# Performance work log

Hardware: AMD Instinct MI355X
Metric: run time of the kernel (lower is better)

## Reference

```python
import jax, jax.numpy as jnp
import numpy as np

# Hyperparameters from __init__ defaults / chosen init kwargs
GAMMA_NEG = 4.0
GAMMA_POS = 1.0
CLIP = 0.05
EPS = 1e-8
ALPHA1 = 2.0
ALPHA_OTHER = 0.5
TOP_K = 10

B, C = 2048, 9605


def setup_inputs() -> dict:
    key = jax.random.key(0)
    k_x, k_y, k_c, k_r, k_d, k_o = jax.random.split(key, 6)
    x = jax.random.normal(k_x, (B, C), dtype=jnp.float32)
    y = (jax.random.uniform(k_y, (B, C)) < 0.01).astype(jnp.float32)
    compost_idx = jax.random.randint(k_c, (30,), 0, C, dtype=jnp.int32)
    recycle_idx = jax.random.randint(k_r, (70,), 0, C, dtype=jnp.int32)
    donate_idx = jax.random.randint(k_d, (70,), 0, C, dtype=jnp.int32)
    other_idx = jax.random.randint(k_o, (40,), 0, C, dtype=jnp.int32)
    # dense whitelist mapping: 0 = not in W_human mapping; priority compost>recycle>donate
    wl_map = jnp.zeros((C,), dtype=jnp.int32)
    wl_map = wl_map.at[other_idx].set(4)
    wl_map = wl_map.at[donate_idx].set(3)
    wl_map = wl_map.at[recycle_idx].set(2)
    wl_map = wl_map.at[compost_idx].set(1)
    return {"x": x, "y": y, "compost_idx": compost_idx,
            "recycle_idx": recycle_idx, "donate_idx": donate_idx,
            "wl_map": wl_map}


def reference(x, y, compost_idx, recycle_idx, donate_idx, wl_map):
    b, c = x.shape
    xs_pos = jax.nn.sigmoid(x)
    xs_neg = jnp.minimum(1.0 - xs_pos + CLIP, 1.0)  # clip shift, clamp max=1
    # base asymmetric BCE term: y*log(p) + (1-y)*log(1-p+clip)
    base = (y * jnp.log(jnp.maximum(xs_pos, EPS))
            + (1.0 - y) * jnp.log(jnp.maximum(xs_neg, EPS)))  # [B, C]

    # per-sample ground-truth whitelist groups (find_gt_whitelist)
    has1 = jnp.sum(y[:, compost_idx], axis=1) > 0  # [B]
    has2 = jnp.sum(y[:, recycle_idx], axis=1) > 0
    has3 = jnp.sum(y[:, donate_idx], axis=1) > 0
    gt_only4 = ~(has1 | has2 | has3)  # gt_whitelist == [4]

    # top-10 predicted classes (argsort descending, first 10)
    _, top_idx = jax.lax.top_k(xs_pos, TOP_K)  # [B, 10]
    rows = jnp.arange(b)

    def step(carry, j):
        # j: [B] class index at current rank; sequential over rank (order matters)
        mult, found = carry
        wl = wl_map[j]                      # group id of this class, 0 if unmapped
        in_map = wl > 0
        in_gt = (((wl == 1) & has1) | ((wl == 2) & has2)
                 | ((wl == 3) & has3) | ((wl == 4) & gt_only4))
        f = jnp.where(in_map & gt_only4, ALPHA_OTHER, 1.0)
        f = f * jnp.where(in_map & (~in_gt) & (~found), ALPHA1, 1.0)
        mult = mult.at[rows, j].multiply(f)
        found = found | (in_map & in_gt)
        return (mult, found), None

    init = (jnp.ones((b, c), x.dtype), jnp.zeros((b,), dtype=bool))
    (mult, found), _ = jax.lax.scan(step, init, top_idx.T)  # scan over 10 ranks

    # if no gt-whitelist match found in top-10: multiply all top-10 by alpha1 again
    extra = jnp.where(found[:, None], 1.0, ALPHA1)  # [B, 1]
    mult = mult.at[rows[:, None], top_idx].multiply(
        jnp.broadcast_to(extra, (b, TOP_K)))

    # asymmetric focal weighting (computed without grad in original)
    pt = xs_pos * y + xs_neg * (1.0 - y)
    gamma = GAMMA_POS * y + GAMMA_NEG * (1.0 - y)
    w = jax.lax.stop_gradient(jnp.power(1.0 - pt, gamma))

    return -jnp.sum(base * mult * w)
```

## Files before the change

### kernel.cpp

```cpp
#include <hip/hip_runtime.h>

#define TOPK 10
#define CLIP 0.05f
#define EPSV 1e-8f
#define ALPHA1 2.0f
#define ALPHA_OTHER 0.5f
#define TCAND 2.5f
#define MAXC 128

__device__ __forceinline__ unsigned long long pack_vc(float v, int c, int C) {
  unsigned u = __float_as_uint(v);
  unsigned key = (u & 0x80000000u) ? ~u : (u | 0x80000000u);
  return ((unsigned long long)key << 32) | (unsigned)(C - c);
}
__device__ __forceinline__ float unpack_v(unsigned long long p) {
  unsigned key = (unsigned)(p >> 32);
  unsigned u = (key & 0x80000000u) ? (key & 0x7fffffffu) : ~key;
  return __uint_as_float(u);
}
__device__ __forceinline__ int unpack_c(unsigned long long p, int C) {
  return C - (int)(unsigned)(p & 0xffffffffu);
}

__device__ __forceinline__ float base_w(float xv, bool pos) {
  float e = __expf(-xv);
  float p = __builtin_amdgcn_rcpf(1.f + e);
  float xneg = fminf(1.f - p + CLIP, 1.f);
  float q = pos ? p : xneg;
  float b = __logf(fmaxf(q, EPSV));
  float t = 1.f - q;
  float t2 = t * t;
  float w = pos ? t : t2 * t2;
  return b * w;
}

__device__ __forceinline__ void push_cand(float v, long flat, int C, double invC,
                                          int* __restrict__ cnt,
                                          unsigned long long* __restrict__ cand,
                                          int maxc) {
  int row = (int)((double)flat * invC);
  int col = (int)(flat - (long)row * (long)C);
  if (col >= C) { row++; col -= C; }
  if (col < 0)  { row--; col += C; }
  int i = atomicAdd(&cnt[row], 1);
  if (i < maxc) cand[(long)row * maxc + i] = pack_vc(v, col, C);
}

__device__ __forceinline__ void proc4(float4 X, float4 Y, float4& acc,
                                      unsigned& cmask, int slot) {
  acc.x += base_w(X.x, Y.x > 0.5f);
  acc.y += base_w(X.y, Y.y > 0.5f);
  acc.z += base_w(X.z, Y.z > 0.5f);
  acc.w += base_w(X.w, Y.w > 0.5f);
  float mx = fmaxf(fmaxf(X.x, X.y), fmaxf(X.z, X.w));
  cmask |= (mx > TCAND ? 1u : 0u) << slot;
}

__global__ __launch_bounds__(256) void stream_kernel(
    const float* __restrict__ x, const float* __restrict__ y,
    float* __restrict__ out, int* __restrict__ cnt,
    unsigned long long* __restrict__ cand, long N, int C, double invC, int maxc)
{
  const long N4 = N >> 2;
  const long S = (long)gridDim.x * 256;
  const long gtid = (long)blockIdx.x * 256 + threadIdx.x;
  const float4* __restrict__ x4 = (const float4*)x;
  const float4* __restrict__ y4 = (const float4*)y;

  float4 a0 = make_float4(0.f, 0.f, 0.f, 0.f);
  float4 a1 = make_float4(0.f, 0.f, 0.f, 0.f);
  float4 a2 = make_float4(0.f, 0.f, 0.f, 0.f);
  float4 a3 = make_float4(0.f, 0.f, 0.f, 0.f);
  unsigned cmask = 0;

  int k = 0;
  long i = gtid;
  for (; i + 3 * S < N4; i += 4 * S, k += 4) {
    float4 X0 = x4[i];         float4 Y0 = y4[i];
    float4 X1 = x4[i + S];     float4 Y1 = y4[i + S];
    float4 X2 = x4[i + 2 * S]; float4 Y2 = y4[i + 2 * S];
    float4 X3 = x4[i + 3 * S]; float4 Y3 = y4[i + 3 * S];
    proc4(X0, Y0, a0, cmask, k + 0);
    proc4(X1, Y1, a1, cmask, k + 1);
    proc4(X2, Y2, a2, cmask, k + 2);
    proc4(X3, Y3, a3, cmask, k + 3);
  }
  for (; i < N4; i += S, k++) {
    float4 X = x4[i]; float4 Y = y4[i];
    proc4(X, Y, a0, cmask, k);
  }
  float sum = (a0.x + a0.y + a0.z + a0.w) + (a1.x + a1.y + a1.z + a1.w)
            + (a2.x + a2.y + a2.z + a2.w) + (a3.x + a3.y + a3.z + a3.w);
  if (gtid == 0) {
    for (long j = N4 * 4; j < N; j++) {
      float xv = x[j];
      sum += base_w(xv, y[j] > 0.5f);
      if (xv > TCAND) push_cand(xv, j, C, invC, cnt, cand, maxc);
    }
  }

  while (cmask) {
    int b = __ffs(cmask) - 1;
    cmask &= cmask - 1;
    long ii = gtid + (long)b * S;
    float4 X = x4[ii];
    long fb = 4 * ii;
    if (X.x > TCAND) push_cand(X.x, fb + 0, C, invC, cnt, cand, maxc);
    if (X.y > TCAND) push_cand(X.y, fb + 1, C, invC, cnt, cand, maxc);
    if (X.z > TCAND) push_cand(X.z, fb + 2, C, invC, cnt, cand, maxc);
    if (X.w > TCAND) push_cand(X.w, fb + 3, C, invC, cnt, cand, maxc);
  }

#pragma unroll
  for (int off = 32; off > 0; off >>= 1) sum += __shfl_xor(sum, off, 64);
  __shared__ float s_sum[4];
  const int lane = threadIdx.x & 63, wave = threadIdx.x >> 6;
  if (lane == 0) s_sum[wave] = sum;
  __syncthreads();
  if (threadIdx.x == 0)
    atomicAdd(out, -(s_sum[0] + s_sum[1] + s_sum[2] + s_sum[3]));
}

__global__ __launch_bounds__(256) void fix_kernel(
    const float* __restrict__ x, const float* __restrict__ y,
    const int* __restrict__ compost, const int* __restrict__ recycle,
    const int* __restrict__ donate, const int* __restrict__ wl_map,
    float* __restrict__ out, const int* __restrict__ cnt,
    const unsigned long long* __restrict__ cand,
    int C, int n1, int n2, int n3, int maxc)
{
  const int row = blockIdx.x;
  const float* xr = x + (size_t)row * (size_t)C;
  const float* yr = y + (size_t)row * (size_t)C;
  const int tid = threadIdx.x;
  const int lane = tid & 63;
  const int wave = tid >> 6;

  __shared__ int s_has[3];
  __shared__ unsigned long long s_top[TOPK];

  if (tid < 3) s_has[tid] = 0;
  __syncthreads();

  const int ntot = n1 + n2 + n3;
  if (wave > 0) {
    for (int i = tid - 64; i < ntot; i += 192) {
      int which, colI;
      if (i < n1)           { which = 0; colI = compost[i]; }
      else if (i < n1 + n2) { which = 1; colI = recycle[i - n1]; }
      else                  { which = 2; colI = donate[i - n1 - n2]; }
      if (yr[colI] > 0.5f) s_has[which] = 1;
    }
  }

  if (wave == 0) {
    const int c = cnt[row];
    unsigned long long ls[TOPK];
#pragma unroll
    for (int s = 0; s < TOPK; s++) ls[s] = 0ULL;

#define INSERT(P)                                                          \
    do {                                                                   \
      unsigned long long _p = (P);                                         \
      if (_p > ls[TOPK - 1]) {                                             \
        _Pragma("unroll")                                                  \
        for (int _s = 0; _s < TOPK; _s++) {                                \
          bool _g = _p > ls[_s];                                           \
          unsigned long long _t = _g ? ls[_s] : _p;                        \
          ls[_s] = _g ? _p : ls[_s];                                       \
          _p = _t;                                                         \
        }                                                                  \
      }                                                                    \
    } while (0)

    if (c >= TOPK && c <= maxc) {
      const unsigned long long* cr = cand + (long)row * maxc;
      for (int i = lane; i < c; i += 64) INSERT(cr[i]);
    } else {
      for (int col = lane; col < C; col += 64) INSERT(pack_vc(xr[col], col, C));
    }
#undef INSERT

    for (int r = 0; r < TOPK; r++) {
      unsigned long long mine = ls[0];
      unsigned long long best = mine;
#pragma unroll
      for (int off = 32; off > 0; off >>= 1) {
        unsigned long long o = __shfl_xor(best, off, 64);
        best = (o > best) ? o : best;
      }
      if (lane == 0) s_top[r] = best;
      if (mine == best) {
#pragma unroll
        for (int s = 0; s < TOPK - 1; s++) ls[s] = ls[s + 1];
        ls[TOPK - 1] = 0ULL;
      }
    }
  }
  __syncthreads();

  if (tid == 0) {
    const bool h1 = s_has[0] != 0, h2 = s_has[1] != 0, h3 = s_has[2] != 0;
    const bool gt4 = !(h1 || h2 || h3);

    bool found = false;
    float fr[TOPK];
#pragma unroll
    for (int r = 0; r < TOPK; r++) {
      int col = unpack_c(s_top[r], C);
      int wl = wl_map[col];
      bool in_map = wl > 0;
      bool in_gt = (wl == 1 && h1) || (wl == 2 && h2) ||
                   (wl == 3 && h3) || (wl == 4 && gt4);
      float f = 1.f;
      if (in_map && gt4) f *= ALPHA_OTHER;
      if (in_map && !in_gt && !found) f *= ALPHA1;
      fr[r] = f;
      found = found || (in_map && in_gt);
    }
    const float extra = found ? 1.f : ALPHA1;
    float total = 0.f;
#pragma unroll
    for (int r = 0; r < TOPK; r++) {
      float mult = fr[r] * extra;
      if (mult != 1.f) {
        int col = unpack_c(s_top[r], C);
        float xv = unpack_v(s_top[r]);
        total += (mult - 1.f) * base_w(xv, yr[col] > 0.5f);
      }
    }
    if (total != 0.f) atomicAdd(out, -total);
  }
}

extern "C" void kernel_launch(void* const* d_in, const int* in_sizes, int n_in,
                              void* d_out, int out_size, void* d_ws, size_t ws_size,
                              hipStream_t stream) {
  const float* x       = (const float*)d_in[0];
  const float* y       = (const float*)d_in[1];
  const int*   compost = (const int*)d_in[2];
  const int*   recycle = (const int*)d_in[3];
  const int*   donate  = (const int*)d_in[4];
  const int*   wl_map  = (const int*)d_in[5];
  float* out = (float*)d_out;

  const int C  = in_sizes[5];
  const int B  = in_sizes[0] / C;
  const long N = (long)in_sizes[0];
  const int n1 = in_sizes[2], n2 = in_sizes[3], n3 = in_sizes[4];

  size_t cand_off = ((size_t)B * 4 + 7) & ~(size_t)7;
  int maxc = MAXC;
  if (ws_size < cand_off + (size_t)B * maxc * 8) {
    size_t fit = (ws_size > cand_off) ? (ws_size - cand_off) / ((size_t)B * 8) : 0;
    maxc = (int)fit;
  }
  int* cnt = (int*)d_ws;
  unsigned long long* cand = (unsigned long long*)((char*)d_ws + cand_off);
  double invC = 1.0 / (double)C;

  long N4 = N >> 2;
  long g = (N4 + 256L * 8 - 1) / (256L * 8);
  if (g < 256) g = 256;
  if (g > 16384) g = 16384;

  hipMemsetAsync(out, 0, sizeof(float), stream);
  hipMemsetAsync(cnt, 0, (size_t)B * 4, stream);
  stream_kernel<<<(int)g, 256, 0, stream>>>(x, y, out, cnt, cand, N, C, invC, maxc);
  fix_kernel<<<B, 256, 0, stream>>>(x, y, compost, recycle, donate, wl_map,
                                    out, cnt, cand, C, n1, n2, n3, maxc);
}
```

Measured before the change: 242.6 us.

## Stream inputs via direct global-to-LDS async loads with per-wave prefetch

```diff
diff --git a/kernel.cpp b/kernel.cpp
--- a/kernel.cpp
+++ b/kernel.cpp
@@ -7,6 +7,16 @@
 #define ALPHA_OTHER 0.5f
 #define TCAND 2.5f
 #define MAXC 128
+
+#define AS1 __attribute__((address_space(1)))
+#define AS3 __attribute__((address_space(3)))
+
+__device__ __forceinline__ void gl_lds16(const void* g, void* l) {
+  __builtin_amdgcn_global_load_lds((AS1 void*)(size_t)g, (AS3 void*)(size_t)l,
+                                   16, 0, 0);
+}
+#define WAIT_VM2() __builtin_amdgcn_s_waitcnt(0x0F72)
+#define WAIT_VM0() __builtin_amdgcn_s_waitcnt(0x0F70)
 
 __device__ __forceinline__ unsigned long long pack_vc(float v, int c, int C) {
   unsigned u = __float_as_uint(v);
@@ -46,76 +56,95 @@
   if (i < maxc) cand[(long)row * maxc + i] = pack_vc(v, col, C);
 }
 
-__device__ __forceinline__ void proc4(float4 X, float4 Y, float4& acc,
-                                      unsigned& cmask, int slot) {
-  acc.x += base_w(X.x, Y.x > 0.5f);
-  acc.y += base_w(X.y, Y.y > 0.5f);
-  acc.z += base_w(X.z, Y.z > 0.5f);
-  acc.w += base_w(X.w, Y.w > 0.5f);
-  float mx = fmaxf(fmaxf(X.x, X.y), fmaxf(X.z, X.w));
-  cmask |= (mx > TCAND ? 1u : 0u) << slot;
-}
-
 __global__ __launch_bounds__(256) void stream_kernel(
     const float* __restrict__ x, const float* __restrict__ y,
     float* __restrict__ out, int* __restrict__ cnt,
     unsigned long long* __restrict__ cand, long N, int C, double invC, int maxc)
 {
   const long N4 = N >> 2;
-  const long S = (long)gridDim.x * 256;
-  const long gtid = (long)blockIdx.x * 256 + threadIdx.x;
+  const long nstage = N4 >> 6;
+  const int lane = threadIdx.x & 63;
+  const int wv = threadIdx.x >> 6;
+  const long w = (long)blockIdx.x * 4 + wv;
+  const long W = (long)gridDim.x * 4;
+
   const float4* __restrict__ x4 = (const float4*)x;
   const float4* __restrict__ y4 = (const float4*)y;
 
-  float4 a0 = make_float4(0.f, 0.f, 0.f, 0.f);
-  float4 a1 = make_float4(0.f, 0.f, 0.f, 0.f);
-  float4 a2 = make_float4(0.f, 0.f, 0.f, 0.f);
-  float4 a3 = make_float4(0.f, 0.f, 0.f, 0.f);
+  __shared__ float4 sbuf[4][4][2][64];
+
+  float4 acc = make_float4(0.f, 0.f, 0.f, 0.f);
   unsigned cmask = 0;
-
-  int k = 0;
-  long i = gtid;
-  for (; i + 3 * S < N4; i += 4 * S, k += 4) {
-    float4 X0 = x4[i];         float4 Y0 = y4[i];
-    float4 X1 = x4[i + S];     float4 Y1 = y4[i + S];
-    float4 X2 = x4[i + 2 * S]; float4 Y2 = y4[i + 2 * S];
-    float4 X3 = x4[i + 3 * S]; float4 Y3 = y4[i + 3 * S];
-    proc4(X0, Y0, a0, cmask, k + 0);
-    proc4(X1, Y1, a1, cmask, k + 1);
-    proc4(X2, Y2, a2, cmask, k + 2);
-    proc4(X3, Y3, a3, cmask, k + 3);
-  }
-  for (; i < N4; i += S, k++) {
-    float4 X = x4[i]; float4 Y = y4[i];
-    proc4(X, Y, a0, cmask, k);
-  }
-  float sum = (a0.x + a0.y + a0.z + a0.w) + (a1.x + a1.y + a1.z + a1.w)
-            + (a2.x + a2.y + a2.z + a2.w) + (a3.x + a3.y + a3.z + a3.w);
-  if (gtid == 0) {
-    for (long j = N4 * 4; j < N; j++) {
-      float xv = x[j];
-      sum += base_w(xv, y[j] > 0.5f);
-      if (xv > TCAND) push_cand(xv, j, C, invC, cnt, cand, maxc);
-    }
-  }
+  float sum = 0.f;
+
+  const int R = (w < nstage) ? (int)((nstage - w + W - 1) / W) : 0;
+
+  if (R > 0) {
+    gl_lds16(x4 + (w << 6) + lane, &sbuf[0][wv][0][0]);
+    gl_lds16(y4 + (w << 6) + lane, &sbuf[0][wv][1][0]);
+  }
+  if (R > 1) {
+    long s1 = w + W;
+    gl_lds16(x4 + (s1 << 6) + lane, &sbuf[1][wv][0][0]);
+    gl_lds16(y4 + (s1 << 6) + lane, &sbuf[1][wv][1][0]);
+  }
+  for (int r = 0; r < R; r++) {
+    const int b = r & 3;
+    if (r + 2 < R) WAIT_VM2(); else WAIT_VM0();
+    float4 X = sbuf[b][wv][0][lane];
+    float4 Y = sbuf[b][wv][1][lane];
+    if (r + 2 < R) {
+      long s2 = w + (long)(r + 2) * W;
+      gl_lds16(x4 + (s2 << 6) + lane, &sbuf[(r + 2) & 3][wv][0][0]);
+      gl_lds16(y4 + (s2 << 6) + lane, &sbuf[(r + 2) & 3][wv][1][0]);
+    }
+    acc.x += base_w(X.x, Y.x > 0.5f);
+    acc.y += base_w(X.y, Y.y > 0.5f);
+    acc.z += base_w(X.z, Y.z > 0.5f);
+    acc.w += base_w(X.w, Y.w > 0.5f);
+    float mx = fmaxf(fmaxf(X.x, X.y), fmaxf(X.z, X.w));
+    cmask |= (mx > TCAND ? 1u : 0u) << r;
+  }
+  sum = acc.x + acc.y + acc.z + acc.w;
 
   while (cmask) {
-    int b = __ffs(cmask) - 1;
+    int r = __ffs((int)cmask) - 1;
     cmask &= cmask - 1;
-    long ii = gtid + (long)b * S;
-    float4 X = x4[ii];
-    long fb = 4 * ii;
+    long i4 = ((w + (long)r * W) << 6) + lane;
+    float4 X = x4[i4];
+    long fb = i4 << 2;
     if (X.x > TCAND) push_cand(X.x, fb + 0, C, invC, cnt, cand, maxc);
     if (X.y > TCAND) push_cand(X.y, fb + 1, C, invC, cnt, cand, maxc);
     if (X.z > TCAND) push_cand(X.z, fb + 2, C, invC, cnt, cand, maxc);
     if (X.w > TCAND) push_cand(X.w, fb + 3, C, invC, cnt, cand, maxc);
   }
 
+  if (blockIdx.x == 0 && wv == 0) {
+    long base4 = nstage << 6;
+    if (base4 + lane < N4) {
+      float4 X = x4[base4 + lane];
+      float4 Y = y4[base4 + lane];
+      long fb = (base4 + lane) << 2;
+      sum += base_w(X.x, Y.x > 0.5f) + base_w(X.y, Y.y > 0.5f)
+           + base_w(X.z, Y.z > 0.5f) + base_w(X.w, Y.w > 0.5f);
+      if (X.x > TCAND) push_cand(X.x, fb + 0, C, invC, cnt, cand, maxc);
+      if (X.y > TCAND) push_cand(X.y, fb + 1, C, invC, cnt, cand, maxc);
+      if (X.z > TCAND) push_cand(X.z, fb + 2, C, invC, cnt, cand, maxc);
+      if (X.w > TCAND) push_cand(X.w, fb + 3, C, invC, cnt, cand, maxc);
+    }
+    if (lane == 0) {
+      for (long j = N4 * 4; j < N; j++) {
+        float xv = x[j];
+        sum += base_w(xv, y[j] > 0.5f);
+        if (xv > TCAND) push_cand(xv, j, C, invC, cnt, cand, maxc);
+      }
+    }
+  }
+
 #pragma unroll
   for (int off = 32; off > 0; off >>= 1) sum += __shfl_xor(sum, off, 64);
   __shared__ float s_sum[4];
-  const int lane = threadIdx.x & 63, wave = threadIdx.x >> 6;
-  if (lane == 0) s_sum[wave] = sum;
+  if (lane == 0) s_sum[wv] = sum;
   __syncthreads();
   if (threadIdx.x == 0)
     atomicAdd(out, -(s_sum[0] + s_sum[1] + s_sum[2] + s_sum[3]));
@@ -259,14 +288,9 @@
   unsigned long long* cand = (unsigned long long*)((char*)d_ws + cand_off);
   double invC = 1.0 / (double)C;
 
-  long N4 = N >> 2;
-  long g = (N4 + 256L * 8 - 1) / (256L * 8);
-  if (g < 256) g = 256;
-  if (g > 16384) g = 16384;
-
   hipMemsetAsync(out, 0, sizeof(float), stream);
   hipMemsetAsync(cnt, 0, (size_t)B * 4, stream);
-  stream_kernel<<<(int)g, 256, 0, stream>>>(x, y, out, cnt, cand, N, C, invC, maxc);
+  stream_kernel<<<1280, 256, 0, stream>>>(x, y, out, cnt, cand, N, C, invC, maxc);
   fix_kernel<<<B, 256, 0, stream>>>(x, y, compost, recycle, donate, wl_map,
                                     out, cnt, cand, C, n1, n2, n3, maxc);
 }
```

After: 242.1 us. About the same (-0.2%).
